# Kernel tuning notes

Hardware: AMD Instinct MI355X
Metric: run time of the kernel (lower is better)

## Reference

```python
import jax, jax.numpy as jnp
import numpy as np

HALF_LOG_2PI = 0.9189385332046727  # 0.5*log(2*pi)


def _sum_layer(prod, logits):
    # prod: [B, R, KK] child log-probs; logits: [R, KK, K] unnormalized sum weights
    W = jax.nn.softmax(logits, axis=1)            # normalized mixture weights
    m = jnp.max(prod, axis=-1, keepdims=True)     # stable logsumexp via einsum
    e = jnp.exp(prod - m)                         # [B, R, KK]
    s = jnp.einsum('brc,rck->brk', e, W)          # [B, R, K]
    return jnp.log(s) + m


def setup_inputs() -> dict:
    key = jax.random.key(0)
    ks = jax.random.split(key, 12)
    B, F, K = 8192, 256, 8
    inp = {
        'x': jax.random.normal(ks[0], (B, F), dtype=jnp.float32),
        'mu': jax.random.normal(ks[1], (F, K), dtype=jnp.float32),
        'log_sigma': jax.random.uniform(ks[2], (F, K), dtype=jnp.float32),
    }
    R = F // 2
    for i in range(8):
        inp['w%d' % i] = jax.random.normal(ks[3 + i], (R, K * K, K), dtype=jnp.float32)
        R //= 2
    inp['root_w'] = jax.random.normal(ks[11], (K,), dtype=jnp.float32)
    return inp


def reference(x, mu, log_sigma, w0, w1, w2, w3, w4, w5, w6, w7, root_w):
    # Gaussian leaf log-probs: [B, F, K]
    z = (x[:, :, None] - mu) * jnp.exp(-log_sigma)
    h = -0.5 * z * z - log_sigma - HALF_LOG_2PI
    # Alternating product (pair adjacent regions) / sum (mix KK -> K) layers
    for w in (w0, w1, w2, w3, w4, w5, w6, w7):
        B, R, K = h.shape
        prod = (h[:, 0::2, :, None] + h[:, 1::2, None, :]).reshape(B, R // 2, K * K)
        h = _sum_layer(prod, w)
    # Root sum node over the K dists of the single remaining region -> [B]
    lp = h[:, 0, :] + jax.nn.log_softmax(root_w)
    return jax.scipy.special.logsumexp(lp, axis=-1)
```

## Files before the change

### kernel.cpp

```cpp
#include <hip/hip_runtime.h>
#include <math.h>

#define NTH 256

static constexpr float HLP = 0.9189385332046727f;

typedef __attribute__((ext_vector_type(2))) _Float16 half2v;
typedef __attribute__((ext_vector_type(2))) __fp16   fp16x2;

static constexpr int L3MF = 524288;
static constexpr size_t WS_NEED_B = (size_t)655360 * 4;

__device__ __forceinline__ half2v pkrtz(float a, float b) {
  return __builtin_bit_cast(half2v, __builtin_amdgcn_cvt_pkrtz(a, b));
}
__device__ __forceinline__ half2v u2h(unsigned u) {
  return __builtin_bit_cast(half2v, u);
}
__device__ __forceinline__ unsigned h2u(half2v h) {
  return __builtin_bit_cast(unsigned, h);
}
__device__ __forceinline__ float dd(half2v a, half2v b, float c) {
#if __has_builtin(__builtin_amdgcn_fdot2)
  return __builtin_amdgcn_fdot2(__builtin_bit_cast(fp16x2, a),
                                __builtin_bit_cast(fp16x2, b), c, false);
#else
  return fmaf((float)a[0], (float)b[0], fmaf((float)a[1], (float)b[1], c));
#endif
}
__device__ __forceinline__ float max8(const float* s) {
  float m = s[0];
  #pragma unroll
  for (int k = 1; k < 8; ++k) m = fmaxf(m, s[k]);
  return m;
}

__device__ __forceinline__ void leaf_ii(float xv, const float* mu8, const float* A8,
                                        const float* B8, half2v* ii, float* M) {
  float h[8];
  float m = -3.0e38f;
  #pragma unroll
  for (int k = 0; k < 8; ++k) {
    const float z = (xv - mu8[k]) * A8[k];
    h[k] = fmaf(-0.5f * z, z, B8[k]);
    m = fmaxf(m, h[k]);
  }
  #pragma unroll
  for (int k = 0; k < 8; ++k) {
    const float n = __expf(h[k] - m);
    ii[k] = pkrtz(n, n);
  }
  *M = m;
}
__device__ __forceinline__ void leaf_pk(float xv, const float* mu8, const float* A8,
                                        const float* B8, half2v* pk, float* M) {
  float h[8];
  float m = -3.0e38f;
  #pragma unroll
  for (int k = 0; k < 8; ++k) {
    const float z = (xv - mu8[k]) * A8[k];
    h[k] = fmaf(-0.5f * z, z, B8[k]);
    m = fmaxf(m, h[k]);
  }
  #pragma unroll
  for (int p = 0; p < 4; ++p) {
    const float n0 = __expf(h[2 * p] - m);
    const float n1 = __expf(h[2 * p + 1] - m);
    pk[p] = pkrtz(n0, n1);
  }
  *M = m;
}

template<int G, bool OUT_II>
__device__ __forceinline__ void combine_d2(const uint4* __restrict__ WL,
                                           const half2v (&na)[G][8],
                                           const half2v (&nb)[G][4],
                                           half2v (&oii)[G][8],
                                           half2v (&opk)[G][4],
                                           float (&M)[G]) {
  float s[G][8];
  #pragma unroll
  for (int g = 0; g < G; ++g)
    #pragma unroll
    for (int k = 0; k < 8; ++k) s[g][k] = 0.f;

  #pragma unroll
  for (int i = 0; i < 8; ++i) {
    half2v e[G][4];
    #pragma unroll
    for (int g = 0; g < G; ++g) {
      e[g][0] = na[g][i] * nb[g][0];
      e[g][1] = na[g][i] * nb[g][1];
      e[g][2] = na[g][i] * nb[g][2];
      e[g][3] = na[g][i] * nb[g][3];
    }
    #pragma unroll
    for (int k = 0; k < 8; ++k) {
      const uint4 w = WL[i * 8 + k];
      #pragma unroll
      for (int g = 0; g < G; ++g) {
        float acc = s[g][k];
        acc = dd(e[g][0], u2h(w.x), acc);
        acc = dd(e[g][1], u2h(w.y), acc);
        acc = dd(e[g][2], u2h(w.z), acc);
        acc = dd(e[g][3], u2h(w.w), acc);
        s[g][k] = acc;
      }
    }
  }
  #pragma unroll
  for (int g = 0; g < G; ++g) {
    const float smax = max8(s[g]);
    const float inv = 1.0f / smax;
    if constexpr (OUT_II) {
      #pragma unroll
      for (int p = 0; p < 8; ++p) {
        const float n = s[g][p] * inv;
        oii[g][p] = pkrtz(n, n);
      }
    } else {
      #pragma unroll
      for (int p = 0; p < 4; ++p)
        opk[g][p] = pkrtz(s[g][2 * p] * inv, s[g][2 * p + 1] * inv);
    }
    M[g] += __logf(smax);
  }
}

__device__ __forceinline__ void prep_col_std(const float* stage, unsigned* wdwL,
                                             int r, int k) {
  float v[64];
  float m = -3.0e38f;
  #pragma unroll
  for (int c = 0; c < 64; ++c) { v[c] = stage[r * 512 + c * 8 + k]; m = fmaxf(m, v[c]); }
  float t = 0.f;
  #pragma unroll
  for (int c = 0; c < 64; ++c) { v[c] = __expf(v[c] - m); t += v[c]; }
  const float inv = 1.0f / t;
  #pragma unroll
  for (int i = 0; i < 8; ++i)
    #pragma unroll
    for (int jp = 0; jp < 4; ++jp)
      wdwL[r * 256 + (i * 8 + k) * 4 + jp] =
          h2u(pkrtz(v[i * 8 + 2 * jp] * inv, v[i * 8 + 2 * jp + 1] * inv));
}

template<bool OUT_II>
__device__ __forceinline__ void subtree_eval(const uint4* __restrict__ wsh4, int sub,
                                             const float* lsh, float4 xv,
                                             half2v (&oii)[1][8], half2v (&opk)[1][4],
                                             float* Mout) {
  half2v ii[1][8], pk[1][4];
  half2v aii[1][8], bpk[1][4];
  half2v dii[1][8], dpk[1][4];
  float Ma, Mb;
  const int fl = 4 * sub;

  leaf_ii(xv.x, lsh + fl * 8,       lsh + 128 + fl * 8,       lsh + 256 + fl * 8,       ii[0], &Ma);
  leaf_pk(xv.y, lsh + (fl + 1) * 8, lsh + 128 + (fl + 1) * 8, lsh + 256 + (fl + 1) * 8, pk[0], &Mb);
  float MA[1] = {Ma + Mb};
  combine_d2<1, true>(wsh4 + (2 * sub) * 64, ii, pk, aii, dpk, MA);

  leaf_ii(xv.z, lsh + (fl + 2) * 8, lsh + 128 + (fl + 2) * 8, lsh + 256 + (fl + 2) * 8, ii[0], &Ma);
  leaf_pk(xv.w, lsh + (fl + 3) * 8, lsh + 128 + (fl + 3) * 8, lsh + 256 + (fl + 3) * 8, pk[0], &Mb);
  float MB[1] = {Ma + Mb};
  combine_d2<1, false>(wsh4 + (2 * sub + 1) * 64, ii, pk, dii, bpk, MB);

  float M[1] = {MA[0] + MB[0]};
  combine_d2<1, OUT_II>(wsh4 + (8 + sub) * 64, aii, bpk, oii, opk, M);
  *Mout = M[0];
}

__global__ __launch_bounds__(NTH, 2) void spn_ab(
    const float* __restrict__ x,
    const float* __restrict__ mu,
    const float* __restrict__ ls,
    const float* __restrict__ w0, const float* __restrict__ w1,
    const float* __restrict__ w2, const float* __restrict__ w3,
    float* __restrict__ ws)
{
  __shared__ float stage[7680];
  __shared__ uint4 wsh4[960];
  __shared__ float lsh[384];
  const int tid = threadIdx.x;
  const int r3 = blockIdx.x >> 5;
  const int chunk = blockIdx.x & 31;

  #pragma unroll
  for (int i = 0; i < 30; ++i) {
    const int idx = tid + 256 * i;
    const int reg = idx >> 9, off = idx & 511;
    const float* src;
    if (reg < 8)       src = w0 + (8 * r3 + reg) * 512;
    else if (reg < 12) src = w1 + (4 * r3 + (reg - 8)) * 512;
    else if (reg < 14) src = w2 + (2 * r3 + (reg - 12)) * 512;
    else               src = w3 + r3 * 512;
    stage[idx] = src[off];
  }
  if (tid < 128) {
    const int base = r3 * 128;
    const float l = ls[base + tid];
    lsh[tid]       = mu[base + tid];
    lsh[128 + tid] = __expf(-l);
    lsh[256 + tid] = -l - HLP;
  }
  __syncthreads();

  if (tid < 120) prep_col_std(stage, reinterpret_cast<unsigned*>(wsh4), tid >> 3, tid & 7);
  __syncthreads();

  const int b = chunk * 256 + tid;
  const float* xb = x + (size_t)b * 256 + 16 * r3;
  const float4 xv0 = *reinterpret_cast<const float4*>(xb);
  const float4 xv1 = *reinterpret_cast<const float4*>(xb + 4);
  const float4 xv2 = *reinterpret_cast<const float4*>(xb + 8);
  const float4 xv3 = *reinterpret_cast<const float4*>(xb + 12);

  half2v s0ii[1][8], s1pk[1][4], s2ii[1][8], s3pk[1][4];
  half2v dii[1][8], dpk[1][4];
  float M0, M1, M2, M3;

  subtree_eval<true >(wsh4, 0, lsh, xv0, s0ii, dpk, &M0);
  subtree_eval<false>(wsh4, 1, lsh, xv1, dii, s1pk, &M1);
  float MA[1] = {M0 + M1};
  half2v cAii[1][8];
  combine_d2<1, true>(wsh4 + 12 * 64, s0ii, s1pk, cAii, dpk, MA);

  subtree_eval<true >(wsh4, 2, lsh, xv2, s2ii, dpk, &M2);
  subtree_eval<false>(wsh4, 3, lsh, xv3, dii, s3pk, &M3);
  float MB[1] = {M2 + M3};
  half2v cBpk[1][4];
  combine_d2<1, false>(wsh4 + 13 * 64, s2ii, s3pk, dii, cBpk, MB);

  float M[1] = {MA[0] + MB[0]};
  half2v n[1][4];
  combine_d2<1, false>(wsh4 + 14 * 64, cAii, cBpk, dii, n, M);

  reinterpret_cast<uint4*>(ws)[r3 * 8192 + b] =
      uint4{h2u(n[0][0]), h2u(n[0][1]), h2u(n[0][2]), h2u(n[0][3])};
  ws[L3MF + r3 * 8192 + b] = M[0];
}

__device__ __forceinline__ float macTd(const uint4* __restrict__ Wr, int myk,
                                       const float* na, const half2v* nbpk) {
  float s = 0.f;
  #pragma unroll
  for (int i = 0; i < 8; ++i) {
    const uint4 w = Wr[myk * 8 + ((i ^ myk) & 7)];
    float T = dd(nbpk[0], u2h(w.x), 0.f);
    T = dd(nbpk[1], u2h(w.y), T);
    T = dd(nbpk[2], u2h(w.z), T);
    T = dd(nbpk[3], u2h(w.w), T);
    s = fmaf(na[i], T, s);
  }
  return s;
}

__global__ __launch_bounds__(NTH) void spn_c(
    const float* __restrict__ w4, const float* __restrict__ w5,
    const float* __restrict__ w6, const float* __restrict__ w7,
    const float* __restrict__ root_w,
    float* __restrict__ ws,
    float* __restrict__ out)
{
  __shared__ float stage[7680];
  __shared__ uint4 wsh4[960];
  __shared__ float ssh[8];
  const int tid = threadIdx.x;

  #pragma unroll
  for (int i = 0; i < 30; ++i) {
    const int idx = tid + 256 * i;
    const int reg = idx >> 9, off = idx & 511;
    const float* src;
    if (reg < 8)       src = w4 + reg * 512;
    else if (reg < 12) src = w5 + (reg - 8) * 512;
    else if (reg < 14) src = w6 + (reg - 12) * 512;
    else               src = w7;
    stage[idx] = src[off];
  }
  if (tid == 255) {
    float m = -3.0e38f;
    for (int k = 0; k < 8; ++k) m = fmaxf(m, root_w[k]);
    float e[8]; float t = 0.f;
    for (int k = 0; k < 8; ++k) { e[k] = __expf(root_w[k] - m); t += e[k]; }
    const float inv = 1.0f / t;
    for (int k = 0; k < 8; ++k) ssh[k] = e[k] * inv;
  }
  __syncthreads();

  if (tid < 120) {
    const int reg = tid >> 3, k = tid & 7;
    float v[64];
    float m = -3.0e38f;
    #pragma unroll
    for (int c = 0; c < 64; ++c) { v[c] = stage[reg * 512 + c * 8 + k]; m = fmaxf(m, v[c]); }
    float t = 0.f;
    #pragma unroll
    for (int c = 0; c < 64; ++c) { v[c] = __expf(v[c] - m); t += v[c]; }
    const float inv = 1.0f / t;
    unsigned* wdwL = reinterpret_cast<unsigned*>(wsh4);
    #pragma unroll
    for (int i = 0; i < 8; ++i)
      #pragma unroll
      for (int jp = 0; jp < 4; ++jp)
        wdwL[reg * 256 + k * 32 + (((i ^ k) & 7) << 2) + jp] =
            h2u(pkrtz(v[i * 8 + 2 * jp] * inv, v[i * 8 + 2 * jp + 1] * inv));
  }
  __syncthreads();

  const int lane = tid & 63, wid = tid >> 6;
  const int myk = lane & 7, bsub = lane >> 3, gbase = lane & 56;
  const int b = blockIdx.x * 32 + wid * 8 + bsub;

  const uint4* n4 = reinterpret_cast<const uint4*>(ws);

  float n4v[8], M4[8];
  #pragma unroll
  for (int r = 0; r < 8; ++r) {
    const uint4 pa = n4[(2 * r + 0) * 8192 + b];
    const uint4 pb = n4[(2 * r + 1) * 8192 + b];
    const float Ma = ws[L3MF + (2 * r + 0) * 8192 + b];
    const float Mb = ws[L3MF + (2 * r + 1) * 8192 + b];
    float na[8];
    const half2v a0 = u2h(pa.x), a1 = u2h(pa.y), a2 = u2h(pa.z), a3 = u2h(pa.w);
    na[0] = (float)a0[0]; na[1] = (float)a0[1];
    na[2] = (float)a1[0]; na[3] = (float)a1[1];
    na[4] = (float)a2[0]; na[5] = (float)a2[1];
    na[6] = (float)a3[0]; na[7] = (float)a3[1];
    half2v nbpk[4] = {u2h(pb.x), u2h(pb.y), u2h(pb.z), u2h(pb.w)};
    float s = macTd(wsh4 + r * 64, myk, na, nbpk);
    float m = s;
    m = fmaxf(m, __shfl_xor(m, 1)); m = fmaxf(m, __shfl_xor(m, 2)); m = fmaxf(m, __shfl_xor(m, 4));
    n4v[r] = s / m;
    M4[r] = Ma + Mb + __logf(m);
  }

  float n5v[4], M5[4];
  #pragma unroll
  for (int r = 0; r < 4; ++r) {
    float na[8]; half2v nbpk[4];
    #pragma unroll
    for (int i = 0; i < 8; ++i) na[i] = __shfl(n4v[2 * r], gbase + i, 64);
    #pragma unroll
    for (int p = 0; p < 4; ++p)
      nbpk[p] = pkrtz(__shfl(n4v[2 * r + 1], gbase + 2 * p, 64),
                      __shfl(n4v[2 * r + 1], gbase + 2 * p + 1, 64));
    float s = macTd(wsh4 + (8 + r) * 64, myk, na, nbpk);
    float m = s;
    m = fmaxf(m, __shfl_xor(m, 1)); m = fmaxf(m, __shfl_xor(m, 2)); m = fmaxf(m, __shfl_xor(m, 4));
    n5v[r] = s / m;
    M5[r] = M4[2 * r] + M4[2 * r + 1] + __logf(m);
  }

  float n6v[2], M6[2];
  #pragma unroll
  for (int r = 0; r < 2; ++r) {
    float na[8]; half2v nbpk[4];
    #pragma unroll
    for (int i = 0; i < 8; ++i) na[i] = __shfl(n5v[2 * r], gbase + i, 64);
    #pragma unroll
    for (int p = 0; p < 4; ++p)
      nbpk[p] = pkrtz(__shfl(n5v[2 * r + 1], gbase + 2 * p, 64),
                      __shfl(n5v[2 * r + 1], gbase + 2 * p + 1, 64));
    float s = macTd(wsh4 + (12 + r) * 64, myk, na, nbpk);
    float m = s;
    m = fmaxf(m, __shfl_xor(m, 1)); m = fmaxf(m, __shfl_xor(m, 2)); m = fmaxf(m, __shfl_xor(m, 4));
    n6v[r] = s / m;
    M6[r] = M5[2 * r] + M5[2 * r + 1] + __logf(m);
  }

  {
    float na[8]; half2v nbpk[4];
    #pragma unroll
    for (int i = 0; i < 8; ++i) na[i] = __shfl(n6v[0], gbase + i, 64);
    #pragma unroll
    for (int p = 0; p < 4; ++p)
      nbpk[p] = pkrtz(__shfl(n6v[1], gbase + 2 * p, 64),
                      __shfl(n6v[1], gbase + 2 * p + 1, 64));
    float s = macTd(wsh4 + 14 * 64, myk, na, nbpk);
    float m = s;
    m = fmaxf(m, __shfl_xor(m, 1)); m = fmaxf(m, __shfl_xor(m, 2)); m = fmaxf(m, __shfl_xor(m, 4));
    const float n7 = s / m;
    const float M7 = M6[0] + M6[1] + __logf(m);
    float prod = n7 * ssh[myk];
    prod += __shfl_xor(prod, 1); prod += __shfl_xor(prod, 2); prod += __shfl_xor(prod, 4);
    if (myk == 0) out[b] = M7 + __logf(prod);
  }
}

static constexpr int NW   = 130560;
static constexpr int AOFF = NW;
static constexpr int BOFF = NW + 2048;
static constexpr int ROFF = NW + 4096;

__device__ __forceinline__ void leaf_eval(float xv, const float* mu8, const float* A8,
                                          const float* B8, float* n, float* M) {
  float h[8];
  float m = -3.0e38f;
  #pragma unroll
  for (int k = 0; k < 8; ++k) {
    const float z = (xv - mu8[k]) * A8[k];
    h[k] = fmaf(-0.5f * z, z, B8[k]);
    m = fmaxf(m, h[k]);
  }
  #pragma unroll
  for (int k = 0; k < 8; ++k) n[k] = __expf(h[k] - m);
  *M = m;
}

__global__ __launch_bounds__(256) void spn_prep(
    const float* __restrict__ ls,
    const float* __restrict__ w0, const float* __restrict__ w1,
    const float* __restrict__ w2, const float* __restrict__ w3,
    const float* __restrict__ w4, const float* __restrict__ w5,
    const float* __restrict__ w6, const float* __restrict__ w7,
    const float* __restrict__ root_w,
    float* __restrict__ ws)
{
  const int job = blockIdx.x * blockDim.x + threadIdx.x;
  if (job < 2040) {
    const float* wl[8] = {w0, w1, w2, w3, w4, w5, w6, w7};
    int j = job, l = 0, base = 0, R = 128;
    while (j >= R * 8) { j -= R * 8; base += R * 512; R >>= 1; ++l; }
    const int r = j >> 3, k = j & 7;
    const float* src = wl[l] + r * 512 + k;
    float v[64];
    float m = -3.0e38f;
    #pragma unroll
    for (int c = 0; c < 64; ++c) { v[c] = src[c * 8]; m = fmaxf(m, v[c]); }
    float ssum = 0.f;
    #pragma unroll
    for (int c = 0; c < 64; ++c) { v[c] = __expf(v[c] - m); ssum += v[c]; }
    const float inv = 1.0f / ssum;
    float* dst = ws + base + r * 512 + k;
    #pragma unroll
    for (int c = 0; c < 64; ++c) dst[c * 8] = v[c] * inv;
  } else if (job < 2040 + 2048) {
    const int i = job - 2040;
    const float l = ls[i];
    ws[AOFF + i] = __expf(-l);
    ws[BOFF + i] = -l - HLP;
  } else if (job == 2040 + 2048) {
    float m = -3.0e38f;
    for (int k = 0; k < 8; ++k) m = fmaxf(m, root_w[k]);
    float e[8]; float ssum = 0.f;
    for (int k = 0; k < 8; ++k) { e[k] = __expf(root_w[k] - m); ssum += e[k]; }
    const float inv = 1.0f / ssum;
    for (int k = 0; k < 8; ++k) ws[ROFF + k] = e[k] * inv;
  }
}

__device__ __forceinline__ void mac64(const float* __restrict__ Wr,
                                      const float* na, const float* nb,
                                      float* s) {
  #pragma unroll
  for (int k = 0; k < 8; ++k) s[k] = 0.f;
  #pragma unroll
  for (int i = 0; i < 8; ++i) {
    const float ai = na[i];
    #pragma unroll
    for (int j = 0; j < 8; ++j) {
      const float e = ai * nb[j];
      const float4 wA = *reinterpret_cast<const float4*>(Wr + (i * 8 + j) * 8);
      const float4 wB = *reinterpret_cast<const float4*>(Wr + (i * 8 + j) * 8 + 4);
      s[0] = fmaf(e, wA.x, s[0]); s[1] = fmaf(e, wA.y, s[1]);
      s[2] = fmaf(e, wA.z, s[2]); s[3] = fmaf(e, wA.w, s[3]);
      s[4] = fmaf(e, wB.x, s[4]); s[5] = fmaf(e, wB.y, s[5]);
      s[6] = fmaf(e, wB.z, s[6]); s[7] = fmaf(e, wB.w, s[7]);
    }
  }
}

#define TB 8
static constexpr int PLA = 128 * 9 + 5;
static constexpr int PLB = 64 * 9 + 5;
static constexpr int NAO = 0;
static constexpr int NBO = TB * PLA;
static constexpr int MAO = NBO + TB * PLB;
static constexpr int MBO = MAO + TB * 128;
static constexpr int SMEM_F = MBO + TB * 64;

__global__ __launch_bounds__(NTH, 2) void spn_main_fb(
    const float* __restrict__ x,
    const float* __restrict__ mu,
    const float* __restrict__ ws,
    float* __restrict__ out)
{
  const float* leafA = ws + AOFF;
  const float* leafB = ws + BOFF;
  const float* srw   = ws + ROFF;

  __shared__ float smem[SMEM_F];

  const int tid = threadIdx.x;
  const int bB = blockIdx.x * TB;

  {
    const float* W0 = ws;
    for (int it = tid; it < TB * 128; it += NTH) {
      const int bb = it & (TB - 1), r = it >> 3;
      float na[8], nb[8], Ma, Mb;
      const int f0 = 2 * r;
      const float xv0 = x[(bB + bb) * 256 + f0];
      const float xv1 = x[(bB + bb) * 256 + f0 + 1];
      leaf_eval(xv0, mu + f0 * 8, leafA + f0 * 8, leafB + f0 * 8, na, &Ma);
      leaf_eval(xv1, mu + f0 * 8 + 8, leafA + f0 * 8 + 8, leafB + f0 * 8 + 8, nb, &Mb);
      float s[8];
      mac64(W0 + r * 512, na, nb, s);
      const float smax = max8(s);
      const float inv = 1.0f / smax;
      const int ob = NAO + bb * PLA + r * 9;
      #pragma unroll
      for (int k = 0; k < 8; ++k) smem[ob + k] = s[k] * inv;
      smem[MAO + bb * 128 + r] = Ma + Mb + __logf(smax);
    }
  }
  __syncthreads();

  int pinO = NAO, poutO = NBO;
  int MinO = MAO, MoutO = MBO;
  int PLIN = PLA, PLOUT = PLB;
  int Rin = 128;
  const float* Wl = ws + 128 * 512;
  for (int l = 1; l < 7; ++l) {
    const int Rout = Rin >> 1;
    for (int it = tid; it < TB * Rout; it += NTH) {
      const int bb = it & (TB - 1), r = it >> 3;
      float na[8], nb[8];
      const int ia = pinO + bb * PLIN + (2 * r) * 9;
      #pragma unroll
      for (int i = 0; i < 8; ++i) { na[i] = smem[ia + i]; nb[i] = smem[ia + 9 + i]; }
      float s[8];
      mac64(Wl + r * 512, na, nb, s);
      const float smax = max8(s);
      const float inv = 1.0f / smax;
      const int ob = poutO + bb * PLOUT + r * 9;
      #pragma unroll
      for (int k = 0; k < 8; ++k) smem[ob + k] = s[k] * inv;
      smem[MoutO + bb * Rout + r] =
          smem[MinO + bb * Rin + 2 * r] + smem[MinO + bb * Rin + 2 * r + 1] + __logf(smax);
    }
    __syncthreads();
    int t;
    t = pinO; pinO = poutO; poutO = t;
    t = MinO; MinO = MoutO; MoutO = t;
    t = PLIN; PLIN = PLOUT; PLOUT = t;
    Rin = Rout;
    Wl += Rout * 512;
  }

  for (int it = tid; it < TB; it += NTH) {
    const int bb = it;
    float na[8], nb[8];
    const int ia = pinO + bb * PLIN;
    #pragma unroll
    for (int i = 0; i < 8; ++i) { na[i] = smem[ia + i]; nb[i] = smem[ia + 9 + i]; }
    float s[8];
    mac64(Wl, na, nb, s);
    float acc = 0.f;
    #pragma unroll
    for (int k = 0; k < 8; ++k) acc = fmaf(s[k], srw[k], acc);
    out[bB + bb] = smem[MinO + bb * 2] + smem[MinO + bb * 2 + 1] + __logf(acc);
  }
}

extern "C" void kernel_launch(void* const* d_in, const int* in_sizes, int n_in,
                              void* d_out, int out_size, void* d_ws, size_t ws_size,
                              hipStream_t stream) {
  (void)in_sizes; (void)n_in; (void)out_size;
  const float* x      = (const float*)d_in[0];
  const float* mu     = (const float*)d_in[1];
  const float* ls     = (const float*)d_in[2];
  const float* w0     = (const float*)d_in[3];
  const float* w1     = (const float*)d_in[4];
  const float* w2     = (const float*)d_in[5];
  const float* w3     = (const float*)d_in[6];
  const float* w4     = (const float*)d_in[7];
  const float* w5     = (const float*)d_in[8];
  const float* w6     = (const float*)d_in[9];
  const float* w7     = (const float*)d_in[10];
  const float* root_w = (const float*)d_in[11];
  float* ws  = (float*)d_ws;
  float* out = (float*)d_out;

  if (ws_size >= WS_NEED_B) {
    spn_ab<<<512, NTH, 0, stream>>>(x, mu, ls, w0, w1, w2, w3, ws);
    spn_c<<<256, NTH, 0, stream>>>(w4, w5, w6, w7, root_w, ws, out);
  } else {
    spn_prep<<<16, 256, 0, stream>>>(ls, w0, w1, w2, w3, w4, w5, w6, w7, root_w, ws);
    spn_main_fb<<<8192 / TB, NTH, 0, stream>>>(x, mu, ws, out);
  }
}
```

Measured before the change: 50.68 us.

## Split subtree evaluation across waves with LDS exchange and pad softmax staging

The first kernel is restructured so each wave evaluates one of four depth-3 subtrees for four batch rows, instead of every thread walking the whole 16-feature tree for one row. Partial results go through shared memory, and the two upper combine levels then run on 128 and then 64 threads. Separately, the weight staging layout is padded (stride 65) so the per-column softmax reads contiguous rows, avoiding LDS bank conflicts. This trades register pressure and idle threads in the upper levels for fewer weight reads per sample and less per-thread serial work.

```diff
diff --git a/kernel.cpp b/kernel.cpp
--- a/kernel.cpp
+++ b/kernel.cpp
@@ -127,12 +127,13 @@
   }
 }
 
-__device__ __forceinline__ void prep_col_std(const float* stage, unsigned* wdwL,
+__device__ __forceinline__ void prep_col_pad(const float* stage, unsigned* wdwL,
                                              int r, int k) {
+  const float* row = stage + r * 520 + k * 65;
   float v[64];
   float m = -3.0e38f;
   #pragma unroll
-  for (int c = 0; c < 64; ++c) { v[c] = stage[r * 512 + c * 8 + k]; m = fmaxf(m, v[c]); }
+  for (int c = 0; c < 64; ++c) { v[c] = row[c]; m = fmaxf(m, v[c]); }
   float t = 0.f;
   #pragma unroll
   for (int c = 0; c < 64; ++c) { v[c] = __expf(v[c] - m); t += v[c]; }
@@ -145,33 +146,55 @@
           h2u(pkrtz(v[i * 8 + 2 * jp] * inv, v[i * 8 + 2 * jp + 1] * inv));
 }
 
-template<bool OUT_II>
-__device__ __forceinline__ void subtree_eval(const uint4* __restrict__ wsh4, int sub,
-                                             const float* lsh, float4 xv,
-                                             half2v (&oii)[1][8], half2v (&opk)[1][4],
-                                             float* Mout) {
-  half2v ii[1][8], pk[1][4];
-  half2v aii[1][8], bpk[1][4];
-  half2v dii[1][8], dpk[1][4];
+__device__ __forceinline__ void mk_ii(uint4 p, half2v* ii) {
+  const half2v a0 = u2h(p.x), a1 = u2h(p.y), a2 = u2h(p.z), a3 = u2h(p.w);
+  ii[0] = __builtin_shufflevector(a0, a0, 0, 0);
+  ii[1] = __builtin_shufflevector(a0, a0, 1, 1);
+  ii[2] = __builtin_shufflevector(a1, a1, 0, 0);
+  ii[3] = __builtin_shufflevector(a1, a1, 1, 1);
+  ii[4] = __builtin_shufflevector(a2, a2, 0, 0);
+  ii[5] = __builtin_shufflevector(a2, a2, 1, 1);
+  ii[6] = __builtin_shufflevector(a3, a3, 0, 0);
+  ii[7] = __builtin_shufflevector(a3, a3, 1, 1);
+}
+
+__device__ __forceinline__ void subtree_g4(
+    const uint4* __restrict__ wA, const uint4* __restrict__ wB,
+    const uint4* __restrict__ wT,
+    const float* m0, const float* A0, const float* B0,
+    const float4 (&xv)[4],
+    half2v (&opk)[4][4], float (&Mout)[4]) {
+  half2v ii[4][8], pk[4][4];
+  half2v aii[4][8], bpk[4][4];
+  half2v dii[4][8], dpk[4][4];
   float Ma, Mb;
-  const int fl = 4 * sub;
-
-  leaf_ii(xv.x, lsh + fl * 8,       lsh + 128 + fl * 8,       lsh + 256 + fl * 8,       ii[0], &Ma);
-  leaf_pk(xv.y, lsh + (fl + 1) * 8, lsh + 128 + (fl + 1) * 8, lsh + 256 + (fl + 1) * 8, pk[0], &Mb);
-  float MA[1] = {Ma + Mb};
-  combine_d2<1, true>(wsh4 + (2 * sub) * 64, ii, pk, aii, dpk, MA);
-
-  leaf_ii(xv.z, lsh + (fl + 2) * 8, lsh + 128 + (fl + 2) * 8, lsh + 256 + (fl + 2) * 8, ii[0], &Ma);
-  leaf_pk(xv.w, lsh + (fl + 3) * 8, lsh + 128 + (fl + 3) * 8, lsh + 256 + (fl + 3) * 8, pk[0], &Mb);
-  float MB[1] = {Ma + Mb};
-  combine_d2<1, false>(wsh4 + (2 * sub + 1) * 64, ii, pk, dii, bpk, MB);
-
-  float M[1] = {MA[0] + MB[0]};
-  combine_d2<1, OUT_II>(wsh4 + (8 + sub) * 64, aii, bpk, oii, opk, M);
-  *Mout = M[0];
-}
-
-__global__ __launch_bounds__(NTH, 2) void spn_ab(
+  float MA[4], MB[4];
+
+  #pragma unroll
+  for (int g = 0; g < 4; ++g) {
+    leaf_ii(xv[g].x, m0,     A0,     B0,     ii[g], &Ma);
+    leaf_pk(xv[g].y, m0 + 8, A0 + 8, B0 + 8, pk[g], &Mb);
+    MA[g] = Ma + Mb;
+  }
+  combine_d2<4, true>(wA, ii, pk, aii, dpk, MA);
+
+  #pragma unroll
+  for (int g = 0; g < 4; ++g) {
+    leaf_ii(xv[g].z, m0 + 16, A0 + 16, B0 + 16, ii[g], &Ma);
+    leaf_pk(xv[g].w, m0 + 24, A0 + 24, B0 + 24, pk[g], &Mb);
+    MB[g] = Ma + Mb;
+  }
+  combine_d2<4, false>(wB, ii, pk, dii, bpk, MB);
+
+  float M[4];
+  #pragma unroll
+  for (int g = 0; g < 4; ++g) M[g] = MA[g] + MB[g];
+  combine_d2<4, false>(wT, aii, bpk, dii, opk, M);
+  #pragma unroll
+  for (int g = 0; g < 4; ++g) Mout[g] = M[g];
+}
+
+__global__ __launch_bounds__(NTH, 2) void spn_f2(
     const float* __restrict__ x,
     const float* __restrict__ mu,
     const float* __restrict__ ls,
@@ -179,7 +202,7 @@
     const float* __restrict__ w2, const float* __restrict__ w3,
     float* __restrict__ ws)
 {
-  __shared__ float stage[7680];
+  __shared__ __attribute__((aligned(16))) float stage[7800];
   __shared__ uint4 wsh4[960];
   __shared__ float lsh[384];
   const int tid = threadIdx.x;
@@ -195,7 +218,7 @@
     else if (reg < 12) src = w1 + (4 * r3 + (reg - 8)) * 512;
     else if (reg < 14) src = w2 + (2 * r3 + (reg - 12)) * 512;
     else               src = w3 + r3 * 512;
-    stage[idx] = src[off];
+    stage[reg * 520 + (off & 7) * 65 + (off >> 3)] = src[off];
   }
   if (tid < 128) {
     const int base = r3 * 128;
@@ -206,39 +229,85 @@
   }
   __syncthreads();
 
-  if (tid < 120) prep_col_std(stage, reinterpret_cast<unsigned*>(wsh4), tid >> 3, tid & 7);
+  if (tid < 120) prep_col_pad(stage, reinterpret_cast<unsigned*>(wsh4), tid >> 3, tid & 7);
   __syncthreads();
 
-  const int b = chunk * 256 + tid;
-  const float* xb = x + (size_t)b * 256 + 16 * r3;
-  const float4 xv0 = *reinterpret_cast<const float4*>(xb);
-  const float4 xv1 = *reinterpret_cast<const float4*>(xb + 4);
-  const float4 xv2 = *reinterpret_cast<const float4*>(xb + 8);
-  const float4 xv3 = *reinterpret_cast<const float4*>(xb + 12);
-
-  half2v s0ii[1][8], s1pk[1][4], s2ii[1][8], s3pk[1][4];
-  half2v dii[1][8], dpk[1][4];
-  float M0, M1, M2, M3;
-
-  subtree_eval<true >(wsh4, 0, lsh, xv0, s0ii, dpk, &M0);
-  subtree_eval<false>(wsh4, 1, lsh, xv1, dii, s1pk, &M1);
-  float MA[1] = {M0 + M1};
-  half2v cAii[1][8];
-  combine_d2<1, true>(wsh4 + 12 * 64, s0ii, s1pk, cAii, dpk, MA);
-
-  subtree_eval<true >(wsh4, 2, lsh, xv2, s2ii, dpk, &M2);
-  subtree_eval<false>(wsh4, 3, lsh, xv3, dii, s3pk, &M3);
-  float MB[1] = {M2 + M3};
-  half2v cBpk[1][4];
-  combine_d2<1, false>(wsh4 + 13 * 64, s2ii, s3pk, dii, cBpk, MB);
-
-  float M[1] = {MA[0] + MB[0]};
-  half2v n[1][4];
-  combine_d2<1, false>(wsh4 + 14 * 64, cAii, cBpk, dii, n, M);
-
-  reinterpret_cast<uint4*>(ws)[r3 * 8192 + b] =
-      uint4{h2u(n[0][0]), h2u(n[0][1]), h2u(n[0][2]), h2u(n[0][3])};
-  ws[L3MF + r3 * 8192 + b] = M[0];
+  uint4* exN = reinterpret_cast<uint4*>(stage);
+  float* exM = stage + 4096;
+  uint4* ex2N = reinterpret_cast<uint4*>(stage + 5120);
+  float* ex2M = stage + 7168;
+
+  {
+    const int q = tid >> 6;
+    const int u = tid & 63;
+    float4 xv[4];
+    #pragma unroll
+    for (int g = 0; g < 4; ++g)
+      xv[g] = *reinterpret_cast<const float4*>(
+          x + (size_t)(chunk * 256 + u + 64 * g) * 256 + 16 * r3 + 4 * q);
+
+    half2v npk[4][4];
+    float M[4];
+    subtree_g4(wsh4 + (2 * q) * 64, wsh4 + (2 * q + 1) * 64, wsh4 + (8 + q) * 64,
+               lsh + q * 32, lsh + 128 + q * 32, lsh + 256 + q * 32,
+               xv, npk, M);
+
+    #pragma unroll
+    for (int g = 0; g < 4; ++g) {
+      exN[q * 256 + u + 64 * g] =
+          uint4{h2u(npk[g][0]), h2u(npk[g][1]), h2u(npk[g][2]), h2u(npk[g][3])};
+      exM[q * 256 + u + 64 * g] = M[g];
+    }
+  }
+  __syncthreads();
+
+  if (tid < 128) {
+    const int h = tid >> 6, u2 = tid & 63;
+    half2v ii[4][8], pk[4][4], dii[4][8];
+    float M[4];
+    #pragma unroll
+    for (int g = 0; g < 4; ++g) {
+      const int s = u2 + 64 * g;
+      const uint4 pa = exN[(2 * h) * 256 + s];
+      const uint4 pb = exN[(2 * h + 1) * 256 + s];
+      mk_ii(pa, ii[g]);
+      pk[g][0] = u2h(pb.x); pk[g][1] = u2h(pb.y); pk[g][2] = u2h(pb.z); pk[g][3] = u2h(pb.w);
+      M[g] = exM[(2 * h) * 256 + s] + exM[(2 * h + 1) * 256 + s];
+    }
+    half2v n[4][4];
+    combine_d2<4, false>(wsh4 + (12 + h) * 64, ii, pk, dii, n, M);
+    #pragma unroll
+    for (int g = 0; g < 4; ++g) {
+      const int s = u2 + 64 * g;
+      ex2N[h * 256 + s] = uint4{h2u(n[g][0]), h2u(n[g][1]), h2u(n[g][2]), h2u(n[g][3])};
+      ex2M[h * 256 + s] = M[g];
+    }
+  }
+  __syncthreads();
+
+  if (tid < 64) {
+    const int u3 = tid;
+    half2v ii[4][8], pk[4][4], dii[4][8];
+    float M[4];
+    #pragma unroll
+    for (int g = 0; g < 4; ++g) {
+      const int s = u3 + 64 * g;
+      const uint4 pa = ex2N[s];
+      const uint4 pb = ex2N[256 + s];
+      mk_ii(pa, ii[g]);
+      pk[g][0] = u2h(pb.x); pk[g][1] = u2h(pb.y); pk[g][2] = u2h(pb.z); pk[g][3] = u2h(pb.w);
+      M[g] = ex2M[s] + ex2M[256 + s];
+    }
+    half2v n[4][4];
+    combine_d2<4, false>(wsh4 + 14 * 64, ii, pk, dii, n, M);
+    uint4* outn = reinterpret_cast<uint4*>(ws);
+    #pragma unroll
+    for (int g = 0; g < 4; ++g) {
+      const int b = chunk * 256 + u3 + 64 * g;
+      outn[r3 * 8192 + b] = uint4{h2u(n[g][0]), h2u(n[g][1]), h2u(n[g][2]), h2u(n[g][3])};
+      ws[L3MF + r3 * 8192 + b] = M[g];
+    }
+  }
 }
 
 __device__ __forceinline__ float macTd(const uint4* __restrict__ Wr, int myk,
@@ -263,7 +332,7 @@
     float* __restrict__ ws,
     float* __restrict__ out)
 {
-  __shared__ float stage[7680];
+  __shared__ __attribute__((aligned(16))) float stage[7800];
   __shared__ uint4 wsh4[960];
   __shared__ float ssh[8];
   const int tid = threadIdx.x;
@@ -277,7 +346,7 @@
     else if (reg < 12) src = w5 + (reg - 8) * 512;
     else if (reg < 14) src = w6 + (reg - 12) * 512;
     else               src = w7;
-    stage[idx] = src[off];
+    stage[reg * 520 + (off & 7) * 65 + (off >> 3)] = src[off];
   }
   if (tid == 255) {
     float m = -3.0e38f;
@@ -291,10 +360,11 @@
 
   if (tid < 120) {
     const int reg = tid >> 3, k = tid & 7;
+    const float* row = stage + reg * 520 + k * 65;
     float v[64];
     float m = -3.0e38f;
     #pragma unroll
-    for (int c = 0; c < 64; ++c) { v[c] = stage[reg * 512 + c * 8 + k]; m = fmaxf(m, v[c]); }
+    for (int c = 0; c < 64; ++c) { v[c] = row[c]; m = fmaxf(m, v[c]); }
     float t = 0.f;
     #pragma unroll
     for (int c = 0; c < 64; ++c) { v[c] = __expf(v[c] - m); t += v[c]; }
@@ -585,7 +655,7 @@
   float* out = (float*)d_out;
 
   if (ws_size >= WS_NEED_B) {
-    spn_ab<<<512, NTH, 0, stream>>>(x, mu, ls, w0, w1, w2, w3, ws);
+    spn_f2<<<512, NTH, 0, stream>>>(x, mu, ls, w0, w1, w2, w3, ws);
     spn_c<<<256, NTH, 0, stream>>>(w4, w5, w6, w7, root_w, ws, out);
   } else {
     spn_prep<<<16, 256, 0, stream>>>(ls, w0, w1, w2, w3, w4, w5, w6, w7, root_w, ws);
```

Result: no change. 51.36 us (+1.3%).
